# Kernel optimization log

Hardware: AMD Instinct MI355X
Metric: run time of the kernel (lower is better)

The kernel has to match this reference:

```python
import jax, jax.numpy as jnp
import numpy as np

DIM = 3072
NUM_HEADS = 24
HEAD_DIM = DIM // NUM_HEADS        # 128
B = 1
F, H, W = 4, 24, 24
S = F * H * W                      # 2304
EPS = 1e-6
MAX_POS = 1024
C2 = HEAD_DIM // 2                 # 64 rotary channel-pairs per head
CF = C2 - 2 * (C2 // 3)            # 22 pairs for frame axis
CH = C2 // 3                       # 21 pairs each for H and W axes


def rmsnorm(x, g, eps=EPS):
    # fp32 RMSNorm over last dim with affine weight g [DIM]
    xf = x.astype(jnp.float32)
    ms = jnp.mean(xf * xf, axis=-1, keepdims=True)
    return (xf * jax.lax.rsqrt(ms + eps) * g).astype(x.dtype)


def apply_default_rope(x, grid_sizes, freqs):
    # x: [B, S, N, D]; freqs: [1024, C2] angle table; grid_sizes: [B,3] (F,H,W)
    b, s, n, d = x.shape
    gh = grid_sizes[0, 1]
    gw = grid_sizes[0, 2]
    pos = jnp.arange(s)
    fi = pos // (gh * gw)
    hi = (pos % (gh * gw)) // gw
    wi = pos % gw
    # per-position angles, split across (F, H, W) channel groups -> [S, C2]
    theta = jnp.concatenate([
        freqs[fi, :CF],
        freqs[hi, CF:CF + CH],
        freqs[wi, CF + CH:],
    ], axis=-1)
    cos = jnp.cos(theta)[None, :, None, :]
    sin = jnp.sin(theta)[None, :, None, :]
    xp = x.astype(jnp.float32).reshape(b, s, n, d // 2, 2)
    xr, xi = xp[..., 0], xp[..., 1]
    out = jnp.stack([xr * cos - xi * sin, xr * sin + xi * cos], axis=-1)
    return out.reshape(b, s, n, d).astype(x.dtype)


def setup_inputs() -> dict:
    key = jax.random.key(0)
    ks = jax.random.split(key, 10)
    def w(k):
        return jax.random.normal(k, (DIM, DIM), dtype=jnp.float32) * 0.02
    inv = 10000.0 ** (-jnp.arange(C2, dtype=jnp.float32) / C2)
    freqs = jnp.arange(MAX_POS, dtype=jnp.float32)[:, None] * inv[None, :]
    return {
        "x": jax.random.normal(ks[0], (B, S, DIM), dtype=jnp.float32),
        "seq_lens": jnp.full((B,), S, dtype=jnp.int32),
        "grid_sizes": jnp.tile(jnp.array([[F, H, W]], dtype=jnp.int32), (B, 1)),
        "freqs": freqs,
        "wq": w(ks[1]), "bq": jnp.zeros((DIM,), jnp.float32),
        "wk": w(ks[2]), "bk": jnp.zeros((DIM,), jnp.float32),
        "wv": w(ks[3]), "bv": jnp.zeros((DIM,), jnp.float32),
        "wo": w(ks[4]), "bo": jnp.zeros((DIM,), jnp.float32),
        "gq": jnp.ones((DIM,), jnp.float32),
        "gk": jnp.ones((DIM,), jnp.float32),
    }


def reference(x, seq_lens, grid_sizes, freqs, wq, bq, wk, bk, wv, bv, wo, bo, gq, gk):
    b, s = x.shape[:2]
    n, d = NUM_HEADS, HEAD_DIM
    # QKV projections (torch Linear: x @ W.T + b) + fp32 RMSNorm on q, k
    q = rmsnorm(x @ wq.T + bq, gq).reshape(b, s, n, d)
    k = rmsnorm(x @ wk.T + bk, gk).reshape(b, s, n, d)
    v = (x @ wv.T + bv).reshape(b, s, n, d)
    # 3-axis (F,H,W) RoPE on q, k
    q = apply_default_rope(q, grid_sizes, freqs)
    k = apply_default_rope(k, grid_sizes, freqs)
    # non-causal attention with k_lens masking
    scores = jnp.einsum('bqnd,bknd->bnqk', q, k) * (d ** -0.5)
    kmask = jnp.arange(s)[None, :] < seq_lens[:, None]          # [B, S]
    scores = jnp.where(kmask[:, None, None, :], scores, -1e9)
    probs = jax.nn.softmax(scores, axis=-1)
    out = jnp.einsum('bnqk,bknd->bqnd', probs, v).reshape(b, s, n * d)
    return out @ wo.T + bo
```

## Files before the change

kernel.cpp:

```cpp
#include <hip/hip_runtime.h>
#include <hip/hip_bf16.h>
#include <cstdint>

#define S_LEN 2304
#define NDIM  3072
#define NH    24
#define HD    128

typedef unsigned short u16;
typedef __bf16  bf16x8  __attribute__((ext_vector_type(8)));
typedef float   floatx4 __attribute__((ext_vector_type(4)));

__device__ __forceinline__ u16 f2bf(float x) {
  union { float f; unsigned int u; } a; a.f = x;
  unsigned int r = (a.u + 0x7FFFu + ((a.u >> 16) & 1u)) >> 16;
  return (u16)r;
}

__device__ __forceinline__ void async_load16(const void* g, void* l) {
  auto gp = (const __attribute__((address_space(1))) unsigned int*)(unsigned long long)(g);
  auto lp = (__attribute__((address_space(3))) unsigned int*)(unsigned int)(unsigned long long)(l);
  __builtin_amdgcn_global_load_lds(gp, lp, 16, 0, 0);
}

__global__ __launch_bounds__(256) void cvt_all(const float* __restrict__ x,
                                               const float* __restrict__ w0,
                                               const float* __restrict__ w1,
                                               const float* __restrict__ w2,
                                               const float* __restrict__ w3,
                                               u16* __restrict__ xo,
                                               u16* __restrict__ o0,
                                               u16* __restrict__ o1,
                                               u16* __restrict__ o2,
                                               u16* __restrict__ o3) {
  long b = blockIdx.x;
  const float* in; u16* out;
  if (b < 3456) { in = x; out = xo; }
  else {
    long wi = (b - 3456) / 4608;
    b = (b - 3456) % 4608;
    in  = (wi == 0) ? w0 : (wi == 1) ? w1 : (wi == 2) ? w2 : w3;
    out = (wi == 0) ? o0 : (wi == 1) ? o1 : (wi == 2) ? o2 : o3;
  }
  long i = (b * 256 + threadIdx.x) * 8;
  float4 a = *(const float4*)(in + i);
  float4 c = *(const float4*)(in + i + 4);
  union { u16 h[8]; uint4 u; } r;
  r.h[0] = f2bf(a.x); r.h[1] = f2bf(a.y); r.h[2] = f2bf(a.z); r.h[3] = f2bf(a.w);
  r.h[4] = f2bf(c.x); r.h[5] = f2bf(c.y); r.h[6] = f2bf(c.z); r.h[7] = f2bf(c.w);
  *(uint4*)(out + i) = r.u;
}

__device__ __forceinline__ void gemm_core128(const u16* __restrict__ A,
                                             const u16* __restrict__ B,
                                             int bm, int bn,
                                             u16* As, u16* Bs,
                                             floatx4 acc[4][4]) {
  constexpr int K = NDIM;
  const int t = threadIdx.x;
  const int l = t & 63, w = t >> 6;
  const int l15 = l & 15, quad = l >> 4;
  const int wm = (w >> 1) * 64, wn = (w & 1) * 64;

#pragma unroll
  for (int i = 0; i < 4; ++i)
#pragma unroll
    for (int j = 0; j < 4; ++j) acc[i][j] = {0.f, 0.f, 0.f, 0.f};

  for (int kt = 0; kt < K / 64; ++kt) {
    const int k0 = kt * 64;
#pragma unroll
    for (int i = 0; i < 4; ++i) {
      int p = i * 256 + t;
      int r = p >> 3;
      int c = (p & 7) ^ (r & 7);
      async_load16(A + (long)(bm + r) * K + k0 + c * 8, As + p * 8);
      async_load16(B + (long)(bn + r) * K + k0 + c * 8, Bs + p * 8);
    }
    __syncthreads();
#pragma unroll
    for (int kk = 0; kk < 2; ++kk) {
      bf16x8 af[4], bfr[4];
#pragma unroll
      for (int i = 0; i < 4; ++i) {
        int row = wm + i * 16 + l15;
        int cc = kk * 4 + quad;
        af[i] = *(const bf16x8*)(As + (row * 8 + (cc ^ (row & 7))) * 8);
      }
#pragma unroll
      for (int j = 0; j < 4; ++j) {
        int row = wn + j * 16 + l15;
        int cc = kk * 4 + quad;
        bfr[j] = *(const bf16x8*)(Bs + (row * 8 + (cc ^ (row & 7))) * 8);
      }
#pragma unroll
      for (int i = 0; i < 4; ++i)
#pragma unroll
        for (int j = 0; j < 4; ++j)
          acc[i][j] = __builtin_amdgcn_mfma_f32_16x16x32_bf16(af[i], bfr[j], acc[i][j], 0, 0, 0);
    }
    __syncthreads();
  }
}

__global__ __launch_bounds__(256, 2) void gemm_qkv(const u16* __restrict__ A,
                                                   const u16* __restrict__ wq,
                                                   const u16* __restrict__ wk,
                                                   const u16* __restrict__ wv,
                                                   const float* __restrict__ bq,
                                                   const float* __restrict__ bk,
                                                   const float* __restrict__ bv,
                                                   float* __restrict__ qf,
                                                   float* __restrict__ kf,
                                                   u16* __restrict__ vbf) {
  __shared__ u16 As[128 * 64];
  __shared__ u16 Bs[128 * 64];
  const int sel = blockIdx.x / 24;
  const int bn = (blockIdx.x % 24) * 128;
  const int bm = blockIdx.y * 128;
  const u16* Bw = (sel == 0) ? wq : (sel == 1) ? wk : wv;
  const float* bias = (sel == 0) ? bq : (sel == 1) ? bk : bv;

  floatx4 acc[4][4];
  gemm_core128(A, Bw, bm, bn, As, Bs, acc);

  const int t = threadIdx.x;
  const int l = t & 63, w = t >> 6;
  const int l15 = l & 15, quad = l >> 4;
  const int wm = (w >> 1) * 64, wn = (w & 1) * 64;

  if (sel < 2) {
    float* C = sel ? kf : qf;
#pragma unroll
    for (int i = 0; i < 4; ++i) {
      const int gm = bm + wm + i * 16 + quad * 4;
#pragma unroll
      for (int j = 0; j < 4; ++j) {
        const int gn = bn + wn + j * 16 + l15;
        const float bb = bias[gn];
#pragma unroll
        for (int r = 0; r < 4; ++r)
          C[(long)(gm + r) * NDIM + gn] = acc[i][j][r] + bb;
      }
    }
  } else {
#pragma unroll
    for (int i = 0; i < 4; ++i) {
      const int gm = bm + wm + i * 16 + quad * 4;
#pragma unroll
      for (int j = 0; j < 4; ++j) {
        const int gn = bn + wn + j * 16 + l15;
        const float bb = bias[gn];
#pragma unroll
        for (int r = 0; r < 4; ++r)
          vbf[(long)(gm + r) * NDIM + gn] = f2bf(acc[i][j][r] + bb);
      }
    }
  }
}

__global__ __launch_bounds__(256, 2) void gemm_bt(const u16* __restrict__ A,
                                                  const u16* __restrict__ Bw,
                                                  const float* __restrict__ bias,
                                                  float* __restrict__ C) {
  __shared__ u16 As[128 * 64];
  __shared__ u16 Bs[128 * 64];
  const int bm = blockIdx.y * 128;
  const int bn = blockIdx.x * 128;

  floatx4 acc[4][4];
  gemm_core128(A, Bw, bm, bn, As, Bs, acc);

  const int t = threadIdx.x;
  const int l = t & 63, w = t >> 6;
  const int l15 = l & 15, quad = l >> 4;
  const int wm = (w >> 1) * 64, wn = (w & 1) * 64;
#pragma unroll
  for (int i = 0; i < 4; ++i) {
    const int gm = bm + wm + i * 16 + quad * 4;
#pragma unroll
    for (int j = 0; j < 4; ++j) {
      const int gn = bn + wn + j * 16 + l15;
      const float bb = bias[gn];
#pragma unroll
      for (int r = 0; r < 4; ++r)
        C[(long)(gm + r) * NDIM + gn] = acc[i][j][r] + bb;
    }
  }
}

__global__ __launch_bounds__(256) void rmsnorm_rope(const float* __restrict__ qxf,
                                                    const float* __restrict__ kxf,
                                                    const float* __restrict__ gqp,
                                                    const float* __restrict__ gkp,
                                                    const float* __restrict__ freqs,
                                                    const int* __restrict__ gsz,
                                                    u16* __restrict__ qop,
                                                    u16* __restrict__ kop) {
  const int tok = blockIdx.x;
  const int tid = threadIdx.x;
  const float* xf = blockIdx.y ? kxf : qxf;
  const float* g  = blockIdx.y ? gkp : gqp;
  u16* outp       = blockIdx.y ? kop : qop;
  const float* row = xf + (long)tok * NDIM;
  float4 v[3];
  float ss = 0.f;
#pragma unroll
  for (int p = 0; p < 3; ++p) {
    v[p] = ((const float4*)row)[p * 256 + tid];
    ss += v[p].x * v[p].x + v[p].y * v[p].y + v[p].z * v[p].z + v[p].w * v[p].w;
  }
#pragma unroll
  for (int m = 1; m < 64; m <<= 1) ss += __shfl_xor(ss, m);
  __shared__ float red[4];
  if ((tid & 63) == 0) red[tid >> 6] = ss;
  __syncthreads();
  ss = red[0] + red[1] + red[2] + red[3];
  const float scale = rsqrtf(ss * (1.0f / NDIM) + 1e-6f);

  const int gh = gsz[1], gw = gsz[2];
  const int hw = gh * gw;
  const int fi = tok / hw;
  const int hi = (tok % hw) / gw;
  const int wi = tok % gw;
#pragma unroll
  for (int p = 0; p < 3; ++p) {
    const int e0 = (p * 256 + tid) * 4;
    const float4 gg = ((const float4*)g)[p * 256 + tid];
    const int hh = e0 >> 7;
    const int d = e0 & 127;
    const int c0 = d >> 1;
    int pos0 = (c0 < 22) ? fi : ((c0 < 43) ? hi : wi);
    int pos1 = (c0 + 1 < 22) ? fi : ((c0 + 1 < 43) ? hi : wi);
    float th0 = freqs[pos0 * 64 + c0];
    float th1 = freqs[pos1 * 64 + c0 + 1];
    float s0, cc0, s1, cc1;
    __sincosf(th0, &s0, &cc0);
    __sincosf(th1, &s1, &cc1);
    float x0 = v[p].x * scale * gg.x;
    float x1 = v[p].y * scale * gg.y;
    float x2 = v[p].z * scale * gg.z;
    float x3 = v[p].w * scale * gg.w;
    union { u16 h[4]; uint2 u; } o;
    o.h[0] = f2bf(x0 * cc0 - x1 * s0);
    o.h[1] = f2bf(x0 * s0 + x1 * cc0);
    o.h[2] = f2bf(x2 * cc1 - x3 * s1);
    o.h[3] = f2bf(x2 * s1 + x3 * cc1);
    *(uint2*)(outp + ((long)hh * S_LEN + tok) * HD + d) = o.u;
  }
}

__global__ __launch_bounds__(256) void vtrans(const u16* __restrict__ vb,
                                              u16* __restrict__ vt) {
  __shared__ u16 tile[64][66];
  const int c0 = blockIdx.x * 64;
  const int t0 = blockIdx.y * 64;
  const int tid = threadIdx.x;
#pragma unroll
  for (int it = 0; it < 16; ++it) {
    int idx = it * 256 + tid;
    int r = idx >> 6, c = idx & 63;
    tile[r][c] = vb[(long)(t0 + r) * NDIM + c0 + c];
  }
  __syncthreads();
#pragma unroll
  for (int it = 0; it < 16; ++it) {
    int idx = it * 256 + tid;
    int r = idx >> 6, c = idx & 63;
    vt[(long)(c0 + r) * S_LEN + t0 + c] = tile[c][r];
  }
}

__global__ __launch_bounds__(256, 2) void attn_kern(const u16* __restrict__ qb,
                                                    const u16* __restrict__ kb,
                                                    const u16* __restrict__ vt,
                                                    const int* __restrict__ seq_lens,
                                                    u16* __restrict__ ob) {
  __shared__ u16 Kb[2][64 * 128];
  __shared__ u16 Vb[2][128 * 64];
  __shared__ u16 Ps[128 * 64];
  const int b = blockIdx.x;
  const int xcd = b & 7;
  const int slot = b >> 3;
  const int h = xcd * 3 + slot / 18;
  const int qt = slot % 18;
  const int t = threadIdx.x;
  const int l = t & 63, w = t >> 6;
  const int l15 = l & 15, quad = l >> 4;
  const int seqlen = seq_lens[0];
  const float SC2 = 0.12753102543f;

  const u16* kbase = kb + (long)h * S_LEN * HD;
  const u16* vbase = vt + (long)h * HD * S_LEN;

  bf16x8 qfrag[2][4];
#pragma unroll
  for (int i = 0; i < 2; ++i) {
    const u16* qrow = qb + ((long)h * S_LEN + qt * 128 + w * 32 + i * 16 + l15) * HD + quad * 8;
#pragma unroll
    for (int kk = 0; kk < 4; ++kk) qfrag[i][kk] = *(const bf16x8*)(qrow + kk * 32);
  }

  bf16x8 ones;
#pragma unroll
  for (int i = 0; i < 8; ++i) ones[i] = (__bf16)1.0f;

  floatx4 oacc[2][8];
  floatx4 lacc[2];
#pragma unroll
  for (int i = 0; i < 2; ++i) {
#pragma unroll
    for (int j = 0; j < 8; ++j) oacc[i][j] = {0.f, 0.f, 0.f, 0.f};
    lacc[i] = {0.f, 0.f, 0.f, 0.f};
  }

  auto stage = [&](int kt, int buf) {
#pragma unroll
    for (int i = 0; i < 4; ++i) {
      int p = i * 256 + t;
      int rk = p >> 4;
      int ck = (p & 15) ^ (rk & 15);
      async_load16(kbase + ((long)(kt * 64 + rk)) * HD + ck * 8, &Kb[buf][p * 8]);
      int dv = p >> 3;
      int cv = (p & 7) ^ (dv & 7);
      async_load16(vbase + (long)dv * S_LEN + kt * 64 + cv * 8, &Vb[buf][p * 8]);
    }
  };

  stage(0, 0);

  for (int kt = 0; kt < S_LEN / 64; ++kt) {
    const int cur = kt & 1;
    __syncthreads();
    if (kt + 1 < S_LEN / 64) stage(kt + 1, cur ^ 1);

    floatx4 sacc[2][4];
#pragma unroll
    for (int i = 0; i < 2; ++i)
#pragma unroll
      for (int j = 0; j < 4; ++j) sacc[i][j] = {0.f, 0.f, 0.f, 0.f};
#pragma unroll
    for (int kk = 0; kk < 4; ++kk) {
#pragma unroll
      for (int j = 0; j < 4; ++j) {
        int row = j * 16 + l15;
        int cc = kk * 4 + quad;
        bf16x8 bk = *(const bf16x8*)(&Kb[cur][(row * 16 + (cc ^ (row & 15))) * 8]);
        sacc[0][j] = __builtin_amdgcn_mfma_f32_16x16x32_bf16(qfrag[0][kk], bk, sacc[0][j], 0, 0, 0);
        sacc[1][j] = __builtin_amdgcn_mfma_f32_16x16x32_bf16(qfrag[1][kk], bk, sacc[1][j], 0, 0, 0);
      }
    }

    const bool tail = (kt * 64 + 64 > seqlen);
#pragma unroll
    for (int i = 0; i < 2; ++i)
#pragma unroll
      for (int j = 0; j < 4; ++j)
#pragma unroll
        for (int r = 0; r < 4; ++r) {
          float sv = sacc[i][j][r] * SC2;
          if (tail) {
            int col = kt * 64 + j * 16 + l15;
            if (col >= seqlen) sv = -1e30f;
          }
          sacc[i][j][r] = exp2f(sv);
        }

#pragma unroll
    for (int i = 0; i < 2; ++i)
#pragma unroll
      for (int j = 0; j < 4; ++j)
#pragma unroll
        for (int r = 0; r < 4; ++r) {
          int rq = w * 32 + i * 16 + quad * 4 + r;
          int ct = j * 16 + l15;
          int cc = ct >> 3;
          Ps[(rq * 8 + (cc ^ (rq & 7))) * 8 + (ct & 7)] = f2bf(sacc[i][j][r]);
        }

#pragma unroll
    for (int kl = 0; kl < 2; ++kl) {
      bf16x8 ap[2];
#pragma unroll
      for (int i = 0; i < 2; ++i) {
        int row = w * 32 + i * 16 + l15;
        int cc = kl * 4 + quad;
        ap[i] = *(const bf16x8*)(&Ps[(row * 8 + (cc ^ (row & 7))) * 8]);
      }
      lacc[0] = __builtin_amdgcn_mfma_f32_16x16x32_bf16(ap[0], ones, lacc[0], 0, 0, 0);
      lacc[1] = __builtin_amdgcn_mfma_f32_16x16x32_bf16(ap[1], ones, lacc[1], 0, 0, 0);
#pragma unroll
      for (int j = 0; j < 8; ++j) {
        int d = j * 16 + l15;
        int ccv = kl * 4 + quad;
        bf16x8 bv = *(const bf16x8*)(&Vb[cur][(d * 8 + (ccv ^ (d & 7))) * 8]);
        oacc[0][j] = __builtin_amdgcn_mfma_f32_16x16x32_bf16(ap[0], bv, oacc[0][j], 0, 0, 0);
        oacc[1][j] = __builtin_amdgcn_mfma_f32_16x16x32_bf16(ap[1], bv, oacc[1][j], 0, 0, 0);
      }
    }
  }

#pragma unroll
  for (int i = 0; i < 2; ++i) {
    float inv[4];
#pragma unroll
    for (int r = 0; r < 4; ++r) inv[r] = 1.0f / lacc[i][r];
#pragma unroll
    for (int j = 0; j < 8; ++j) {
      int gt = qt * 128 + w * 32 + i * 16 + quad * 4;
      int gc = h * HD + j * 16 + l15;
#pragma unroll
      for (int r = 0; r < 4; ++r)
        ob[(long)(gt + r) * NDIM + gc] = f2bf(oacc[i][j][r] * inv[r]);
    }
  }
}

extern "C" void kernel_launch(void* const* d_in, const int* in_sizes, int n_in,
                              void* d_out, int out_size, void* d_ws, size_t ws_size,
                              hipStream_t stream) {
  const float* x        = (const float*)d_in[0];
  const int*   seq_lens = (const int*)  d_in[1];
  const int*   gsz      = (const int*)  d_in[2];
  const float* freqs    = (const float*)d_in[3];
  const float* wq       = (const float*)d_in[4];
  const float* bq       = (const float*)d_in[5];
  const float* wk       = (const float*)d_in[6];
  const float* bk       = (const float*)d_in[7];
  const float* wv       = (const float*)d_in[8];
  const float* bv       = (const float*)d_in[9];
  const float* wo       = (const float*)d_in[10];
  const float* bo       = (const float*)d_in[11];
  const float* gq       = (const float*)d_in[12];
  const float* gk       = (const float*)d_in[13];
  float* out = (float*)d_out;

  char* ws = (char*)d_ws;
  const size_t SD2 = (size_t)S_LEN * NDIM * 2;
  const size_t W2  = (size_t)NDIM * NDIM * 2;
  const size_t SD4 = (size_t)S_LEN * NDIM * 4;
  size_t off = 0;
  u16* xb    = (u16*)(ws + off); off += SD2;
  u16* wqb   = (u16*)(ws + off); off += W2;
  u16* wkb   = (u16*)(ws + off); off += W2;
  u16* wvb   = (u16*)(ws + off); off += W2;
  u16* wob   = (u16*)(ws + off); off += W2;
  float* qf  = (float*)(ws + off); off += SD4;
  float* kf  = (float*)(ws + off); off += SD4;
  u16* vbf   = (u16*)(ws + off); off += SD4;
  u16* qbuf  = (u16*)(ws + off); off += SD2;
  u16* kbuf  = (u16*)(ws + off); off += SD2;
  u16* vtb   = (u16*)(ws + off); off += SD2;
  u16* attnb = (u16*)(ws + off); off += SD2;

  cvt_all<<<3456 + 4 * 4608, 256, 0, stream>>>(x, wq, wk, wv, wo,
                                               xb, wqb, wkb, wvb, wob);

  gemm_qkv<<<dim3(72, 18), 256, 0, stream>>>(xb, wqb, wkb, wvb,
                                             bq, bk, bv, qf, kf, vbf);

  rmsnorm_rope<<<dim3(S_LEN, 2), 256, 0, stream>>>(qf, kf, gq, gk, freqs, gsz,
                                                   qbuf, kbuf);
  vtrans<<<dim3(NDIM / 64, S_LEN / 64), 256, 0, stream>>>(vbf, vtb);

  attn_kern<<<432, 256, 0, stream>>>(qbuf, kbuf, vtb, seq_lens, attnb);

  gemm_bt<<<dim3(24, 18), 256, 0, stream>>>(attnb, wob, bo, out);
}
```

Baseline: 552.1 us.

## Fuse V transpose into QKV epilogue, enlarge attention tiles, add MFMA priority

The QKV GEMM epilogue now writes V directly in transposed [dim, seq] layout with 8-byte stores, so the separate vtrans kernel and its intermediate buffer go away. The attention kernel moves to 512 threads covering 256 query rows per block, which halves the grid and lets each staged K/V tile serve twice as many queries. s_setprio is raised around the MFMA loops. Risks: the transposed stores from the GEMM are strided and less coalesced, 216 blocks may underfill the CUs, and the larger block increases LDS and register pressure.

```diff
diff --git a/kernel.cpp b/kernel.cpp
--- a/kernel.cpp
+++ b/kernel.cpp
@@ -112,7 +112,7 @@
                                                    const float* __restrict__ bv,
                                                    float* __restrict__ qf,
                                                    float* __restrict__ kf,
-                                                   u16* __restrict__ vbf) {
+                                                   u16* __restrict__ vt) {
   __shared__ u16 As[128 * 64];
   __shared__ u16 Bs[128 * 64];
   const int sel = blockIdx.x / 24;
@@ -151,9 +151,10 @@
       for (int j = 0; j < 4; ++j) {
         const int gn = bn + wn + j * 16 + l15;
         const float bb = bias[gn];
-#pragma unroll
-        for (int r = 0; r < 4; ++r)
-          vbf[(long)(gm + r) * NDIM + gn] = f2bf(acc[i][j][r] + bb);
+        union { u16 h[4]; uint2 u; } o;
+#pragma unroll
+        for (int r = 0; r < 4; ++r) o.h[r] = f2bf(acc[i][j][r] + bb);
+        *(uint2*)(vt + (long)gn * S_LEN + gm) = o.u;
       }
     }
   }
@@ -250,40 +251,19 @@
   }
 }
 
-__global__ __launch_bounds__(256) void vtrans(const u16* __restrict__ vb,
-                                              u16* __restrict__ vt) {
-  __shared__ u16 tile[64][66];
-  const int c0 = blockIdx.x * 64;
-  const int t0 = blockIdx.y * 64;
-  const int tid = threadIdx.x;
-#pragma unroll
-  for (int it = 0; it < 16; ++it) {
-    int idx = it * 256 + tid;
-    int r = idx >> 6, c = idx & 63;
-    tile[r][c] = vb[(long)(t0 + r) * NDIM + c0 + c];
-  }
-  __syncthreads();
-#pragma unroll
-  for (int it = 0; it < 16; ++it) {
-    int idx = it * 256 + tid;
-    int r = idx >> 6, c = idx & 63;
-    vt[(long)(c0 + r) * S_LEN + t0 + c] = tile[c][r];
-  }
-}
-
-__global__ __launch_bounds__(256, 2) void attn_kern(const u16* __restrict__ qb,
+__global__ __launch_bounds__(512, 2) void attn_kern(const u16* __restrict__ qb,
                                                     const u16* __restrict__ kb,
                                                     const u16* __restrict__ vt,
                                                     const int* __restrict__ seq_lens,
                                                     u16* __restrict__ ob) {
   __shared__ u16 Kb[2][64 * 128];
   __shared__ u16 Vb[2][128 * 64];
-  __shared__ u16 Ps[128 * 64];
+  __shared__ u16 Ps[256 * 64];
   const int b = blockIdx.x;
   const int xcd = b & 7;
   const int slot = b >> 3;
-  const int h = xcd * 3 + slot / 18;
-  const int qt = slot % 18;
+  const int h = xcd * 3 + slot / 9;
+  const int qt = slot % 9;
   const int t = threadIdx.x;
   const int l = t & 63, w = t >> 6;
   const int l15 = l & 15, quad = l >> 4;
@@ -296,7 +276,7 @@
   bf16x8 qfrag[2][4];
 #pragma unroll
   for (int i = 0; i < 2; ++i) {
-    const u16* qrow = qb + ((long)h * S_LEN + qt * 128 + w * 32 + i * 16 + l15) * HD + quad * 8;
+    const u16* qrow = qb + ((long)h * S_LEN + qt * 256 + w * 32 + i * 16 + l15) * HD + quad * 8;
 #pragma unroll
     for (int kk = 0; kk < 4; ++kk) qfrag[i][kk] = *(const bf16x8*)(qrow + kk * 32);
   }
@@ -316,8 +296,8 @@
 
   auto stage = [&](int kt, int buf) {
 #pragma unroll
-    for (int i = 0; i < 4; ++i) {
-      int p = i * 256 + t;
+    for (int i = 0; i < 2; ++i) {
+      int p = i * 512 + t;
       int rk = p >> 4;
       int ck = (p & 15) ^ (rk & 15);
       async_load16(kbase + ((long)(kt * 64 + rk)) * HD + ck * 8, &Kb[buf][p * 8]);
@@ -339,6 +319,7 @@
     for (int i = 0; i < 2; ++i)
 #pragma unroll
       for (int j = 0; j < 4; ++j) sacc[i][j] = {0.f, 0.f, 0.f, 0.f};
+    __builtin_amdgcn_s_setprio(1);
 #pragma unroll
     for (int kk = 0; kk < 4; ++kk) {
 #pragma unroll
@@ -350,6 +331,7 @@
         sacc[1][j] = __builtin_amdgcn_mfma_f32_16x16x32_bf16(qfrag[1][kk], bk, sacc[1][j], 0, 0, 0);
       }
     }
+    __builtin_amdgcn_s_setprio(0);
 
     const bool tail = (kt * 64 + 64 > seqlen);
 #pragma unroll
@@ -378,6 +360,7 @@
           Ps[(rq * 8 + (cc ^ (rq & 7))) * 8 + (ct & 7)] = f2bf(sacc[i][j][r]);
         }
 
+    __builtin_amdgcn_s_setprio(1);
 #pragma unroll
     for (int kl = 0; kl < 2; ++kl) {
       bf16x8 ap[2];
@@ -398,6 +381,7 @@
         oacc[1][j] = __builtin_amdgcn_mfma_f32_16x16x32_bf16(ap[1], bv, oacc[1][j], 0, 0, 0);
       }
     }
+    __builtin_amdgcn_s_setprio(0);
   }
 
 #pragma unroll
@@ -407,7 +391,7 @@
     for (int r = 0; r < 4; ++r) inv[r] = 1.0f / lacc[i][r];
 #pragma unroll
     for (int j = 0; j < 8; ++j) {
-      int gt = qt * 128 + w * 32 + i * 16 + quad * 4;
+      int gt = qt * 256 + w * 32 + i * 16 + quad * 4;
       int gc = h * HD + j * 16 + l15;
 #pragma unroll
       for (int r = 0; r < 4; ++r)
@@ -447,23 +431,21 @@
   u16* wob   = (u16*)(ws + off); off += W2;
   float* qf  = (float*)(ws + off); off += SD4;
   float* kf  = (float*)(ws + off); off += SD4;
-  u16* vbf   = (u16*)(ws + off); off += SD4;
+  u16* vtb   = (u16*)(ws + off); off += SD2;
   u16* qbuf  = (u16*)(ws + off); off += SD2;
   u16* kbuf  = (u16*)(ws + off); off += SD2;
-  u16* vtb   = (u16*)(ws + off); off += SD2;
   u16* attnb = (u16*)(ws + off); off += SD2;
 
   cvt_all<<<3456 + 4 * 4608, 256, 0, stream>>>(x, wq, wk, wv, wo,
                                                xb, wqb, wkb, wvb, wob);
 
   gemm_qkv<<<dim3(72, 18), 256, 0, stream>>>(xb, wqb, wkb, wvb,
-                                             bq, bk, bv, qf, kf, vbf);
+                                             bq, bk, bv, qf, kf, vtb);
 
   rmsnorm_rope<<<dim3(S_LEN, 2), 256, 0, stream>>>(qf, kf, gq, gk, freqs, gsz,
                                                    qbuf, kbuf);
-  vtrans<<<dim3(NDIM / 64, S_LEN / 64), 256, 0, stream>>>(vbf, vtb);
-
-  attn_kern<<<432, 256, 0, stream>>>(qbuf, kbuf, vtb, seq_lens, attnb);
+
+  attn_kern<<<216, 512, 0, stream>>>(qbuf, kbuf, vtb, seq_lens, attnb);
 
   gemm_bt<<<dim3(24, 18), 256, 0, stream>>>(attnb, wob, bo, out);
 }
```

Result: faster. 518.3 us (-6.1%).
